# Kernel optimization log

Hardware: AMD Instinct MI355X
Metric: run time of the kernel (lower is better)

The kernel has to match this reference:

```python
import jax, jax.numpy as jnp
import numpy as np

B, G, D = 4096, 512, 64  # batch, n_groups, group_size; total features P = G*D
EPS = 1e-5
NEG_SLOPE = 0.2


def setup_inputs() -> dict:
    key = jax.random.key(0)
    k1, k2, k3 = jax.random.split(key, 3)
    x = jax.random.normal(k1, (B, G * D), dtype=jnp.float32)
    idx = jnp.arange(G * D, dtype=jnp.int64).reshape(G, D)
    # per-group Linear(d, 1, bias=False) weights, stacked -> [G, D]
    W = jax.random.normal(k2, (G, D), dtype=jnp.float32) * (1.0 / np.sqrt(D))
    gamma = jnp.ones((G,), dtype=jnp.float32)
    beta = jnp.zeros((G,), dtype=jnp.float32)
    fc_w = jax.random.normal(k3, (G,), dtype=jnp.float32) * (1.0 / np.sqrt(G))
    fc_b = jnp.zeros((1,), dtype=jnp.float32)
    return {"x": x, "idx": idx, "W": W, "gamma": gamma, "beta": beta,
            "fc_w": fc_w, "fc_b": fc_b}


def reference(x, idx, W, gamma, beta, fc_w, fc_b):
    # per-group gather: x[:, idx] -> [B, G, D]
    xg = jnp.take(x, idx, axis=1)
    # fused per-group Linear(D,1,no bias) + LeakyReLU(0.2) -> [B, G]
    reps = jnp.einsum('bgd,gd->bg', xg, W)
    reps = jnp.where(reps >= 0, reps, NEG_SLOPE * reps)
    # BatchNorm1d (training-mode batch stats, biased variance, eps=1e-5)
    mean = jnp.mean(reps, axis=0)
    var = jnp.mean((reps - mean) ** 2, axis=0)
    y = gamma * (reps - mean) * jax.lax.rsqrt(var + EPS) + beta
    # Linear(G, 1) + sigmoid -> [B, 1]
    logit = y @ fc_w + fc_b  # [B] + [1] broadcast -> [B]
    return jax.nn.sigmoid(logit)[:, None]
```

## Files before the change

### kernel.cpp

```cpp
#include <hip/hip_runtime.h>
#include <math.h>

static constexpr int   kB = 4096;
static constexpr int   kG = 512;
static constexpr int   kD = 64;
static constexpr int   kP = kG * kD;
static constexpr int   kYB = kB / 256;
static constexpr float kEps   = 1e-5f;
static constexpr float kSlope = 0.2f;

template<bool STORE_REPS>
__global__ __launch_bounds__(256) void pass1(const float* __restrict__ x,
                                             const int*   __restrict__ idxw,
                                             const float* __restrict__ W,
                                             float* __restrict__ reps,
                                             float* __restrict__ psum,
                                             float* __restrict__ psumsq) {
    const int tid  = threadIdx.x;
    const int w    = tid >> 6;
    const int lane = tid & 63;
    const int seg  = lane >> 4;
    const int s    = lane & 15;
    const int q    = blockIdx.x;
    const int g    = 4 * q + seg;
    const int base = g * 64 + 4 * s;

    const int wstride = (idxw[1] == 0 && idxw[2] == 1) ? 2 : 1;
    const int f0 = idxw[(size_t)(base + 0) * wstride];
    const int f1 = idxw[(size_t)(base + 1) * wstride];
    const int f2 = idxw[(size_t)(base + 2) * wstride];
    const int f3 = idxw[(size_t)(base + 3) * wstride];
    const bool contig = (f1 == f0 + 1) && (f2 == f0 + 2) && (f3 == f0 + 3) &&
                        ((f0 & 3) == 0);
    const float4 wv = *(const float4*)(W + base);

    const int row0 = blockIdx.y * 256 + w * 64;
    float asum = 0.f, asq = 0.f;

    if (contig) {
        const float4* p = (const float4*)(x + (size_t)row0 * kP + f0);
        float* rp = STORE_REPS ? (reps + (size_t)row0 * kG + g) : nullptr;
        #pragma unroll 4
        for (int i = 0; i < 64; ++i) {
            const float4 xv = *p;
            p += kP / 4;
            float dot = xv.x * wv.x + xv.y * wv.y + xv.z * wv.z + xv.w * wv.w;
            dot += __shfl_xor(dot, 1, 16);
            dot += __shfl_xor(dot, 2, 16);
            dot += __shfl_xor(dot, 4, 16);
            dot += __shfl_xor(dot, 8, 16);
            const float v = dot >= 0.f ? dot : kSlope * dot;
            if (s == 0) {
                if (STORE_REPS) { *rp = v; rp += kG; }
                asum += v; asq += v * v;
            }
        }
    } else {
        #pragma unroll 2
        for (int i = 0; i < 64; ++i) {
            const int b = row0 + i;
            const float* xr = x + (size_t)b * kP;
            float dot = xr[f0] * wv.x + xr[f1] * wv.y + xr[f2] * wv.z +
                        xr[f3] * wv.w;
            dot += __shfl_xor(dot, 1, 16);
            dot += __shfl_xor(dot, 2, 16);
            dot += __shfl_xor(dot, 4, 16);
            dot += __shfl_xor(dot, 8, 16);
            const float v = dot >= 0.f ? dot : kSlope * dot;
            if (s == 0) {
                if (STORE_REPS) reps[(size_t)b * kG + g] = v;
                asum += v; asq += v * v;
            }
        }
    }

    __shared__ float ls[4][4];
    __shared__ float lq[4][4];
    if (s == 0) { ls[w][seg] = asum; lq[w][seg] = asq; }
    __syncthreads();
    if (tid < 4) {
        const int gg = 4 * q + tid;
        psum  [(size_t)blockIdx.y * kG + gg] =
            ls[0][tid] + ls[1][tid] + ls[2][tid] + ls[3][tid];
        psumsq[(size_t)blockIdx.y * kG + gg] =
            lq[0][tid] + lq[1][tid] + lq[2][tid] + lq[3][tid];
    }
}

__global__ __launch_bounds__(kG) void pass2(const float* __restrict__ psum,
                                            const float* __restrict__ psumsq,
                                            const float* __restrict__ gamma,
                                            const float* __restrict__ beta,
                                            const float* __restrict__ fcw,
                                            const float* __restrict__ fcb,
                                            float* __restrict__ acoef,
                                            float* __restrict__ cval) {
    const int g = threadIdx.x;
    float s = 0.f, ss = 0.f;
    #pragma unroll
    for (int y = 0; y < kYB; ++y) {
        s  += psum  [(size_t)y * kG + g];
        ss += psumsq[(size_t)y * kG + g];
    }
    const float invB = 1.0f / (float)kB;
    const float mean = s * invB;
    float var = ss * invB - mean * mean;
    var = var < 0.f ? 0.f : var;
    const float rs = rsqrtf(var + kEps);
    const float fw = fcw[g];
    const float ga = gamma[g];
    acoef[g] = fw * ga * rs;
    float cg = fw * (beta[g] - ga * mean * rs);

    __shared__ float red[kG];
    red[g] = cg;
    __syncthreads();
    for (int off = kG / 2; off > 0; off >>= 1) {
        if (g < off) red[g] += red[g + off];
        __syncthreads();
    }
    if (g == 0) cval[0] = red[0] + fcb[0];
}

__global__ __launch_bounds__(256) void pass3(const float* __restrict__ reps,
                                             const float* __restrict__ acoef,
                                             const float* __restrict__ cval,
                                             float* __restrict__ out) {
    const int tid  = threadIdx.x;
    const int w    = tid >> 6;
    const int lane = tid & 63;
    const int b    = blockIdx.x * 4 + w;
    const float* r = reps + (size_t)b * kG;

    float acc = 0.f;
    #pragma unroll
    for (int c = 0; c < 2; ++c) {
        const int o = c * 256 + lane * 4;
        const float4 rv = *(const float4*)(r + o);
        const float4 av = *(const float4*)(acoef + o);
        acc += rv.x * av.x + rv.y * av.y + rv.z * av.z + rv.w * av.w;
    }
    acc += __shfl_xor(acc, 1, 64);
    acc += __shfl_xor(acc, 2, 64);
    acc += __shfl_xor(acc, 4, 64);
    acc += __shfl_xor(acc, 8, 64);
    acc += __shfl_xor(acc, 16, 64);
    acc += __shfl_xor(acc, 32, 64);
    if (lane == 0) {
        const float logit = acc + cval[0];
        out[b] = 1.f / (1.f + expf(-logit));
    }
}

__global__ __launch_bounds__(256) void pass3_re(const float* __restrict__ x,
                                                const int*   __restrict__ idxw,
                                                const float* __restrict__ W,
                                                const float* __restrict__ acoef,
                                                float* __restrict__ logit) {
    const int tid  = threadIdx.x;
    const int w    = tid >> 6;
    const int lane = tid & 63;
    const int seg  = lane >> 4;
    const int s    = lane & 15;
    const int q    = blockIdx.x;
    const int g    = 4 * q + seg;
    const int base = g * 64 + 4 * s;

    const int wstride = (idxw[1] == 0 && idxw[2] == 1) ? 2 : 1;
    const int f0 = idxw[(size_t)(base + 0) * wstride];
    const int f1 = idxw[(size_t)(base + 1) * wstride];
    const int f2 = idxw[(size_t)(base + 2) * wstride];
    const int f3 = idxw[(size_t)(base + 3) * wstride];
    const float4 wv = *(const float4*)(W + base);
    const float ag = acoef[g];

    const int row0 = blockIdx.y * 256 + w * 64;
    for (int i = 0; i < 64; ++i) {
        const int b = row0 + i;
        const float* xr = x + (size_t)b * kP;
        float dot = xr[f0] * wv.x + xr[f1] * wv.y + xr[f2] * wv.z +
                    xr[f3] * wv.w;
        dot += __shfl_xor(dot, 1, 16);
        dot += __shfl_xor(dot, 2, 16);
        dot += __shfl_xor(dot, 4, 16);
        dot += __shfl_xor(dot, 8, 16);
        const float v = dot >= 0.f ? dot : kSlope * dot;
        float t = (s == 0) ? ag * v : 0.f;
        t += __shfl_xor(t, 16, 64);
        t += __shfl_xor(t, 32, 64);
        if (lane == 0) atomicAdd(&logit[b], t);
    }
}

__global__ __launch_bounds__(256) void pass4(const float* __restrict__ logit,
                                             const float* __restrict__ cval,
                                             float* __restrict__ out) {
    const int b = blockIdx.x * 256 + threadIdx.x;
    const float l = logit[b] + cval[0];
    out[b] = 1.f / (1.f + expf(-l));
}

extern "C" void kernel_launch(void* const* d_in, const int* in_sizes, int n_in,
                              void* d_out, int out_size, void* d_ws,
                              size_t ws_size, hipStream_t stream) {
    const float* x     = (const float*)d_in[0];
    const int*   idxw  = (const int*)  d_in[1];
    const float* W     = (const float*)d_in[2];
    const float* gamma = (const float*)d_in[3];
    const float* beta  = (const float*)d_in[4];
    const float* fcw   = (const float*)d_in[5];
    const float* fcb   = (const float*)d_in[6];
    float* out = (float*)d_out;

    const size_t need_fast =
        ((size_t)kB * kG + (2 * kYB + 1) * (size_t)kG + 16) * sizeof(float);

    if (ws_size >= need_fast) {
        float* reps   = (float*)d_ws;
        float* psum   = reps + (size_t)kB * kG;
        float* psumsq = psum + (size_t)kYB * kG;
        float* acoef  = psumsq + (size_t)kYB * kG;
        float* cval   = acoef + kG;
        pass1<true><<<dim3(kG / 4, kYB), 256, 0, stream>>>(
            x, idxw, W, reps, psum, psumsq);
        pass2<<<1, kG, 0, stream>>>(psum, psumsq, gamma, beta, fcw, fcb,
                                    acoef, cval);
        pass3<<<kB / 4, 256, 0, stream>>>(reps, acoef, cval, out);
    } else {
        float* psum   = (float*)d_ws;
        float* psumsq = psum + (size_t)kYB * kG;
        float* acoef  = psumsq + (size_t)kYB * kG;
        float* cval   = acoef + kG;
        float* logit  = cval + 4;
        hipMemsetAsync(logit, 0, kB * sizeof(float), stream);
        pass1<false><<<dim3(kG / 4, kYB), 256, 0, stream>>>(
            x, idxw, W, nullptr, psum, psumsq);
        pass2<<<1, kG, 0, stream>>>(psum, psumsq, gamma, beta, fcw, fcb,
                                    acoef, cval);
        pass3_re<<<dim3(kG / 4, kYB), 256, 0, stream>>>(
            x, idxw, W, acoef, logit);
        pass4<<<kB / 256, 256, 0, stream>>>(logit, cval, out);
    }
}
```

Baseline: 692.5 us.

## Stream x row-contiguously in pass1 and move batch stats to a separate strip reduction

Pass1 now gives each wave one half-row of x and reads it contiguously with float4 loads, instead of striding across rows 128 KB apart. Identity of the index map is checked once by a small device kernel that sets a flag. The per-group batch statistics move out of pass1 into a new strip kernel that re-reads the reps buffer, followed by a final reduction over 64 strips. This trades a column-strided, poorly coalesced read of the 512 MB x for fully sequential streaming, at the cost of two extra launches and an extra 8 MB read of reps.

After: 717.3 us. +3.6%, slower.

```diff
diff --git a/kernel.cpp b/kernel.cpp
--- a/kernel.cpp
+++ b/kernel.cpp
@@ -6,60 +6,62 @@
 static constexpr int   kD = 64;
 static constexpr int   kP = kG * kD;
 static constexpr int   kYB = kB / 256;
+static constexpr int   kStrips = 64;
 static constexpr float kEps   = 1e-5f;
 static constexpr float kSlope = 0.2f;
 
-template<bool STORE_REPS>
-__global__ __launch_bounds__(256) void pass1(const float* __restrict__ x,
-                                             const int*   __restrict__ idxw,
-                                             const float* __restrict__ W,
-                                             float* __restrict__ reps,
-                                             float* __restrict__ psum,
-                                             float* __restrict__ psumsq) {
+__global__ __launch_bounds__(256) void k_idxcheck(const int* __restrict__ idxw,
+                                                  int* __restrict__ flag) {
+    const int e = blockIdx.x * 256 + threadIdx.x;
+    const int wstride = (idxw[1] == 0 && idxw[2] == 1) ? 2 : 1;
+    bool ok = (idxw[(size_t)e * wstride] == e);
+    if (wstride == 2) ok = ok && (idxw[(size_t)e * 2 + 1] == 0);
+    if (!ok) atomicOr(flag, 1);
+}
+
+__global__ __launch_bounds__(256) void p1_stream(const float* __restrict__ x,
+                                                 const int*   __restrict__ idxw,
+                                                 const float* __restrict__ W,
+                                                 const int*   __restrict__ flag,
+                                                 float* __restrict__ reps) {
     const int tid  = threadIdx.x;
     const int w    = tid >> 6;
     const int lane = tid & 63;
     const int seg  = lane >> 4;
     const int s    = lane & 15;
-    const int q    = blockIdx.x;
-    const int g    = 4 * q + seg;
-    const int base = g * 64 + 4 * s;
-
-    const int wstride = (idxw[1] == 0 && idxw[2] == 1) ? 2 : 1;
-    const int f0 = idxw[(size_t)(base + 0) * wstride];
-    const int f1 = idxw[(size_t)(base + 1) * wstride];
-    const int f2 = idxw[(size_t)(base + 2) * wstride];
-    const int f3 = idxw[(size_t)(base + 3) * wstride];
-    const bool contig = (f1 == f0 + 1) && (f2 == f0 + 2) && (f3 == f0 + 3) &&
-                        ((f0 & 3) == 0);
-    const float4 wv = *(const float4*)(W + base);
-
-    const int row0 = blockIdx.y * 256 + w * 64;
-    float asum = 0.f, asq = 0.f;
-
-    if (contig) {
-        const float4* p = (const float4*)(x + (size_t)row0 * kP + f0);
-        float* rp = STORE_REPS ? (reps + (size_t)row0 * kG + g) : nullptr;
-        #pragma unroll 4
+
+    const int waveG = blockIdx.x * 4 + w;
+    const int row   = waveG >> 1;
+    const int half  = waveG & 1;
+    const int colbase = half * (kP / 2);
+
+    float* rp = reps + (size_t)row * kG + half * (kG / 2);
+
+    if (flag[0] == 0) {
+        const float4* xp = (const float4*)(x + (size_t)row * kP + colbase) + lane;
+        const float4* wp = (const float4*)(W + colbase) + lane;
+        #pragma unroll 8
         for (int i = 0; i < 64; ++i) {
-            const float4 xv = *p;
-            p += kP / 4;
+            const float4 xv = xp[i * 64];
+            const float4 wv = wp[i * 64];
             float dot = xv.x * wv.x + xv.y * wv.y + xv.z * wv.z + xv.w * wv.w;
             dot += __shfl_xor(dot, 1, 16);
             dot += __shfl_xor(dot, 2, 16);
             dot += __shfl_xor(dot, 4, 16);
             dot += __shfl_xor(dot, 8, 16);
             const float v = dot >= 0.f ? dot : kSlope * dot;
-            if (s == 0) {
-                if (STORE_REPS) { *rp = v; rp += kG; }
-                asum += v; asq += v * v;
-            }
+            if (s == 0) rp[i * 4 + seg] = v;
         }
     } else {
-        #pragma unroll 2
+        const int wstride = (idxw[1] == 0 && idxw[2] == 1) ? 2 : 1;
+        const float* xr = x + (size_t)row * kP;
         for (int i = 0; i < 64; ++i) {
-            const int b = row0 + i;
-            const float* xr = x + (size_t)b * kP;
+            const int e = colbase + i * 256 + lane * 4;
+            const int f0 = idxw[(size_t)(e + 0) * wstride];
+            const int f1 = idxw[(size_t)(e + 1) * wstride];
+            const int f2 = idxw[(size_t)(e + 2) * wstride];
+            const int f3 = idxw[(size_t)(e + 3) * wstride];
+            const float4 wv = *(const float4*)(W + e);
             float dot = xr[f0] * wv.x + xr[f1] * wv.y + xr[f2] * wv.z +
                         xr[f3] * wv.w;
             dot += __shfl_xor(dot, 1, 16);
@@ -67,38 +69,43 @@
             dot += __shfl_xor(dot, 4, 16);
             dot += __shfl_xor(dot, 8, 16);
             const float v = dot >= 0.f ? dot : kSlope * dot;
-            if (s == 0) {
-                if (STORE_REPS) reps[(size_t)b * kG + g] = v;
-                asum += v; asq += v * v;
-            }
+            if (s == 0) rp[i * 4 + seg] = v;
         }
     }
-
-    __shared__ float ls[4][4];
-    __shared__ float lq[4][4];
-    if (s == 0) { ls[w][seg] = asum; lq[w][seg] = asq; }
-    __syncthreads();
-    if (tid < 4) {
-        const int gg = 4 * q + tid;
-        psum  [(size_t)blockIdx.y * kG + gg] =
-            ls[0][tid] + ls[1][tid] + ls[2][tid] + ls[3][tid];
-        psumsq[(size_t)blockIdx.y * kG + gg] =
-            lq[0][tid] + lq[1][tid] + lq[2][tid] + lq[3][tid];
-    }
-}
-
-__global__ __launch_bounds__(kG) void pass2(const float* __restrict__ psum,
-                                            const float* __restrict__ psumsq,
-                                            const float* __restrict__ gamma,
-                                            const float* __restrict__ beta,
-                                            const float* __restrict__ fcw,
-                                            const float* __restrict__ fcb,
-                                            float* __restrict__ acoef,
-                                            float* __restrict__ cval) {
+}
+
+__global__ __launch_bounds__(256) void p2_strip(const float* __restrict__ reps,
+                                                float* __restrict__ psum,
+                                                float* __restrict__ psumsq) {
+    const int j = blockIdx.x;
+    const int t = threadIdx.x;
+    #pragma unroll
+    for (int c = 0; c < 2; ++c) {
+        const int g = c * 256 + t;
+        const float* rp = reps + (size_t)j * 64 * kG + g;
+        float s = 0.f, ss = 0.f;
+        #pragma unroll 8
+        for (int r = 0; r < 64; ++r) {
+            const float v = rp[(size_t)r * kG];
+            s += v; ss += v * v;
+        }
+        psum  [(size_t)j * kG + g] = s;
+        psumsq[(size_t)j * kG + g] = ss;
+    }
+}
+
+__global__ __launch_bounds__(kG) void p2_final(const float* __restrict__ psum,
+                                               const float* __restrict__ psumsq,
+                                               const float* __restrict__ gamma,
+                                               const float* __restrict__ beta,
+                                               const float* __restrict__ fcw,
+                                               const float* __restrict__ fcb,
+                                               float* __restrict__ acoef,
+                                               float* __restrict__ cval) {
     const int g = threadIdx.x;
     float s = 0.f, ss = 0.f;
-    #pragma unroll
-    for (int y = 0; y < kYB; ++y) {
+    #pragma unroll 8
+    for (int y = 0; y < kStrips; ++y) {
         s  += psum  [(size_t)y * kG + g];
         ss += psumsq[(size_t)y * kG + g];
     }
@@ -150,6 +157,92 @@
         const float logit = acc + cval[0];
         out[b] = 1.f / (1.f + expf(-logit));
     }
+}
+
+template<bool STORE_REPS>
+__global__ __launch_bounds__(256) void pass1_old(const float* __restrict__ x,
+                                                 const int*   __restrict__ idxw,
+                                                 const float* __restrict__ W,
+                                                 float* __restrict__ reps,
+                                                 float* __restrict__ psum,
+                                                 float* __restrict__ psumsq) {
+    const int tid  = threadIdx.x;
+    const int w    = tid >> 6;
+    const int lane = tid & 63;
+    const int seg  = lane >> 4;
+    const int s    = lane & 15;
+    const int q    = blockIdx.x;
+    const int g    = 4 * q + seg;
+    const int base = g * 64 + 4 * s;
+
+    const int wstride = (idxw[1] == 0 && idxw[2] == 1) ? 2 : 1;
+    const int f0 = idxw[(size_t)(base + 0) * wstride];
+    const int f1 = idxw[(size_t)(base + 1) * wstride];
+    const int f2 = idxw[(size_t)(base + 2) * wstride];
+    const int f3 = idxw[(size_t)(base + 3) * wstride];
+    const float4 wv = *(const float4*)(W + base);
+
+    const int row0 = blockIdx.y * 256 + w * 64;
+    float asum = 0.f, asq = 0.f;
+    #pragma unroll 2
+    for (int i = 0; i < 64; ++i) {
+        const int b = row0 + i;
+        const float* xr = x + (size_t)b * kP;
+        float dot = xr[f0] * wv.x + xr[f1] * wv.y + xr[f2] * wv.z + xr[f3] * wv.w;
+        dot += __shfl_xor(dot, 1, 16);
+        dot += __shfl_xor(dot, 2, 16);
+        dot += __shfl_xor(dot, 4, 16);
+        dot += __shfl_xor(dot, 8, 16);
+        const float v = dot >= 0.f ? dot : kSlope * dot;
+        if (s == 0) {
+            if (STORE_REPS) reps[(size_t)b * kG + g] = v;
+            asum += v; asq += v * v;
+        }
+    }
+    __shared__ float ls[4][4];
+    __shared__ float lq[4][4];
+    if (s == 0) { ls[w][seg] = asum; lq[w][seg] = asq; }
+    __syncthreads();
+    if (tid < 4) {
+        const int gg = 4 * q + tid;
+        psum  [(size_t)blockIdx.y * kG + gg] = ls[0][tid] + ls[1][tid] + ls[2][tid] + ls[3][tid];
+        psumsq[(size_t)blockIdx.y * kG + gg] = lq[0][tid] + lq[1][tid] + lq[2][tid] + lq[3][tid];
+    }
+}
+
+__global__ __launch_bounds__(kG) void pass2_old(const float* __restrict__ psum,
+                                                const float* __restrict__ psumsq,
+                                                const float* __restrict__ gamma,
+                                                const float* __restrict__ beta,
+                                                const float* __restrict__ fcw,
+                                                const float* __restrict__ fcb,
+                                                float* __restrict__ acoef,
+                                                float* __restrict__ cval) {
+    const int g = threadIdx.x;
+    float s = 0.f, ss = 0.f;
+    #pragma unroll
+    for (int y = 0; y < kYB; ++y) {
+        s  += psum  [(size_t)y * kG + g];
+        ss += psumsq[(size_t)y * kG + g];
+    }
+    const float invB = 1.0f / (float)kB;
+    const float mean = s * invB;
+    float var = ss * invB - mean * mean;
+    var = var < 0.f ? 0.f : var;
+    const float rs = rsqrtf(var + kEps);
+    const float fw = fcw[g];
+    const float ga = gamma[g];
+    acoef[g] = fw * ga * rs;
+    float cg = fw * (beta[g] - ga * mean * rs);
+
+    __shared__ float red[kG];
+    red[g] = cg;
+    __syncthreads();
+    for (int off = kG / 2; off > 0; off >>= 1) {
+        if (g < off) red[g] += red[g + off];
+        __syncthreads();
+    }
+    if (g == 0) cval[0] = red[0] + fcb[0];
 }
 
 __global__ __launch_bounds__(256) void pass3_re(const float* __restrict__ x,
@@ -178,8 +271,7 @@
     for (int i = 0; i < 64; ++i) {
         const int b = row0 + i;
         const float* xr = x + (size_t)b * kP;
-        float dot = xr[f0] * wv.x + xr[f1] * wv.y + xr[f2] * wv.z +
-                    xr[f3] * wv.w;
+        float dot = xr[f0] * wv.x + xr[f1] * wv.y + xr[f2] * wv.z + xr[f3] * wv.w;
         dot += __shfl_xor(dot, 1, 16);
         dot += __shfl_xor(dot, 2, 16);
         dot += __shfl_xor(dot, 4, 16);
@@ -213,18 +305,22 @@
     float* out = (float*)d_out;
 
     const size_t need_fast =
-        ((size_t)kB * kG + (2 * kYB + 1) * (size_t)kG + 16) * sizeof(float);
+        ((size_t)kB * kG + 2 * (size_t)kStrips * kG + kG + 8) * sizeof(float);
 
     if (ws_size >= need_fast) {
         float* reps   = (float*)d_ws;
         float* psum   = reps + (size_t)kB * kG;
-        float* psumsq = psum + (size_t)kYB * kG;
-        float* acoef  = psumsq + (size_t)kYB * kG;
+        float* psumsq = psum + (size_t)kStrips * kG;
+        float* acoef  = psumsq + (size_t)kStrips * kG;
         float* cval   = acoef + kG;
-        pass1<true><<<dim3(kG / 4, kYB), 256, 0, stream>>>(
-            x, idxw, W, reps, psum, psumsq);
-        pass2<<<1, kG, 0, stream>>>(psum, psumsq, gamma, beta, fcw, fcb,
-                                    acoef, cval);
+        int*   flag   = (int*)(cval + 4);
+
+        hipMemsetAsync(flag, 0, sizeof(int), stream);
+        k_idxcheck<<<kP / 256, 256, 0, stream>>>(idxw, flag);
+        p1_stream<<<kB * 2 / 4, 256, 0, stream>>>(x, idxw, W, flag, reps);
+        p2_strip<<<kStrips, 256, 0, stream>>>(reps, psum, psumsq);
+        p2_final<<<1, kG, 0, stream>>>(psum, psumsq, gamma, beta, fcw, fcb,
+                                       acoef, cval);
         pass3<<<kB / 4, 256, 0, stream>>>(reps, acoef, cval, out);
     } else {
         float* psum   = (float*)d_ws;
@@ -233,12 +329,11 @@
         float* cval   = acoef + kG;
         float* logit  = cval + 4;
         hipMemsetAsync(logit, 0, kB * sizeof(float), stream);
-        pass1<false><<<dim3(kG / 4, kYB), 256, 0, stream>>>(
+        pass1_old<false><<<dim3(kG / 4, kYB), 256, 0, stream>>>(
             x, idxw, W, nullptr, psum, psumsq);
-        pass2<<<1, kG, 0, stream>>>(psum, psumsq, gamma, beta, fcw, fcb,
-                                    acoef, cval);
-        pass3_re<<<dim3(kG / 4, kYB), 256, 0, stream>>>(
-            x, idxw, W, acoef, logit);
+        pass2_old<<<1, kG, 0, stream>>>(psum, psumsq, gamma, beta, fcw, fcb,
+                                        acoef, cval);
+        pass3_re<<<dim3(kG / 4, kYB), 256, 0, stream>>>(x, idxw, W, acoef, logit);
         pass4<<<kB / 256, 256, 0, stream>>>(logit, cval, out);
     }
 }
```
